# Performance work log

Measured on AMD Instinct MI355X. Metric: run time of the kernel, lower is better.

Reference implementation:

```python
import jax, jax.numpy as jnp
import numpy as np

BETA_MEM = 0.9
BETA_INH = 0.6
THRESHOLD = 1.0  # snn.Leaky default


def setup_inputs() -> dict:
    key = jax.random.key(0)
    k1, = jax.random.split(key, 1)
    T, B = 1024, 16384
    spike_seq = (jax.random.uniform(k1, (T, B, 2)) < 0.05).astype(jnp.float32)
    w_exc = jnp.array([[0.7, 1.0]], dtype=jnp.float32)  # fc_exc.weight, [1, 2]
    w_inh = jnp.array(-1.0, dtype=jnp.float32)          # scalar inhibitory weight
    return {"spike_seq": spike_seq, "w_exc": w_exc, "w_inh": w_inh}


@jax.custom_vjp
def spike_fn(x):
    # Heaviside spike with ATan surrogate gradient (snntorch default, alpha=2)
    return (x > 0).astype(x.dtype)

def _spike_fwd(x):
    return spike_fn(x), x

def _spike_bwd(x, g):
    return (g / (1.0 + (jnp.pi * x) ** 2),)

spike_fn.defvjp(_spike_fwd, _spike_bwd)


def reference(spike_seq, w_exc, w_inh):
    T, B, _ = spike_seq.shape
    mem0 = jnp.zeros((B, 1), dtype=spike_seq.dtype)
    inh0 = jnp.zeros((B, 1), dtype=spike_seq.dtype)

    def step(carry, x_t):
        mem, inh = carry
        cur_exc = x_t @ w_exc.T                      # [B, 1]
        fm1 = x_t[:, 0:1]                            # [B, 1]
        inh = BETA_INH * inh + fm1
        cur = cur_exc + w_inh * inh
        # snn.Leaky: reset (subtract) computed from previous mem, detached
        reset = jax.lax.stop_gradient((mem - THRESHOLD > 0).astype(mem.dtype))
        mem = BETA_MEM * mem + cur - reset * THRESHOLD
        spk = spike_fn(mem - THRESHOLD)
        return (mem, inh), (spk, mem)

    _, (spk_rec, mem_rec) = jax.lax.scan(step, (mem0, inh0), spike_seq)
    return spk_rec, mem_rec  # each [T, B, 1]
```

## Files before the change

kernel.cpp:

```cpp
#include <hip/hip_runtime.h>

#define T_LEN 1024
#define B_N   16384
#define UNROLL 16

__global__ __launch_bounds__(64, 1) void FMFMNeuronInhib_34033320854098_kernel(
    const float* __restrict__ x,
    const float* __restrict__ w_exc,
    const float* __restrict__ w_inh,
    float* __restrict__ out) {
#pragma clang fp contract(off)
  const int b = blockIdx.x * 64 + threadIdx.x;
  const float w0 = w_exc[0];
  const float w1 = w_exc[1];
  const float wi = w_inh[0];

  float* __restrict__ spk_out = out;
  float* __restrict__ mem_out = out + (size_t)T_LEN * B_N;
  const float2* __restrict__ xp = (const float2*)x;

  float mem = 0.0f;
  float inh = 0.0f;

  float2 cur_buf[UNROLL];
  float2 nxt_buf[UNROLL];

#pragma unroll
  for (int u = 0; u < UNROLL; ++u) cur_buf[u] = xp[u * B_N + b];

  for (int t0 = 0; t0 < T_LEN; t0 += UNROLL) {
    const int t1 = t0 + UNROLL;
    if (t1 < T_LEN) {
#pragma unroll
      for (int u = 0; u < UNROLL; ++u) nxt_buf[u] = xp[(t1 + u) * B_N + b];
    }
#pragma unroll
    for (int u = 0; u < UNROLL; ++u) {
      const int t = t0 + u;
      const float x0 = cur_buf[u].x;
      const float x1 = cur_buf[u].y;
      const float cur_exc = x0 * w0 + x1 * w1;
      inh = 0.6f * inh + x0;
      const float cur = cur_exc + wi * inh;
      const float reset = (mem - 1.0f > 0.0f) ? 1.0f : 0.0f;
      mem = 0.9f * mem + cur - reset * 1.0f;
      const float spk = (mem - 1.0f > 0.0f) ? 1.0f : 0.0f;
      spk_out[t * B_N + b] = spk;
      mem_out[t * B_N + b] = mem;
    }
#pragma unroll
    for (int u = 0; u < UNROLL; ++u) cur_buf[u] = nxt_buf[u];
  }
}

extern "C" void kernel_launch(void* const* d_in, const int* in_sizes, int n_in,
                              void* d_out, int out_size, void* d_ws, size_t ws_size,
                              hipStream_t stream) {
  const float* x     = (const float*)d_in[0];
  const float* w_exc = (const float*)d_in[1];
  const float* w_inh = (const float*)d_in[2];
  float* out = (float*)d_out;

  dim3 grid(B_N / 64);
  dim3 block(64);
  hipLaunchKernelGGL(FMFMNeuronInhib_34033320854098_kernel, grid, block, 0, stream,
                     x, w_exc, w_inh, out);
}
```

Baseline: 259.2 us.

## Ping-pong double-buffer input loads with sched barriers and nontemporal stores

Replaces the copy-based prefetch buffer with two alternating register buffers of 32 steps each. The loads for one half are issued before computing the other half, and scheduling barriers pin that order. Outputs are written with nontemporal stores to avoid polluting the cache. This is meant to keep more memory loads in flight per thread and drop the register copy, at the cost of higher register pressure.

```diff
diff --git a/kernel.cpp b/kernel.cpp
--- a/kernel.cpp
+++ b/kernel.cpp
@@ -2,7 +2,7 @@
 
 #define T_LEN 1024
 #define B_N   16384
-#define UNROLL 16
+#define UNROLL 32
 
 __global__ __launch_bounds__(64, 1) void FMFMNeuronInhib_34033320854098_kernel(
     const float* __restrict__ x,
@@ -17,39 +17,52 @@
 
   float* __restrict__ spk_out = out;
   float* __restrict__ mem_out = out + (size_t)T_LEN * B_N;
-  const float2* __restrict__ xp = (const float2*)x;
+  const float2* __restrict__ xp = (const float2*)x + b;
 
   float mem = 0.0f;
   float inh = 0.0f;
 
-  float2 cur_buf[UNROLL];
-  float2 nxt_buf[UNROLL];
+  auto step = [&](int t, float2 xv) {
+#pragma clang fp contract(off)
+    const float x0 = xv.x;
+    const float x1 = xv.y;
+    const float cur_exc = x0 * w0 + x1 * w1;
+    inh = 0.6f * inh + x0;
+    const float cur = cur_exc + wi * inh;
+    const float reset = (mem - 1.0f > 0.0f) ? 1.0f : 0.0f;
+    mem = 0.9f * mem + cur - reset * 1.0f;
+    const float spk = (mem - 1.0f > 0.0f) ? 1.0f : 0.0f;
+    __builtin_nontemporal_store(spk, &spk_out[(size_t)t * B_N + b]);
+    __builtin_nontemporal_store(mem, &mem_out[(size_t)t * B_N + b]);
+  };
+
+  float2 bufA[UNROLL];
+  float2 bufB[UNROLL];
 
 #pragma unroll
-  for (int u = 0; u < UNROLL; ++u) cur_buf[u] = xp[u * B_N + b];
+  for (int u = 0; u < UNROLL; ++u) bufA[u] = xp[(size_t)u * B_N];
+  __builtin_amdgcn_sched_barrier(0);
 
-  for (int t0 = 0; t0 < T_LEN; t0 += UNROLL) {
-    const int t1 = t0 + UNROLL;
-    if (t1 < T_LEN) {
+  for (int t0 = 0; t0 < T_LEN; t0 += 2 * UNROLL) {
 #pragma unroll
-      for (int u = 0; u < UNROLL; ++u) nxt_buf[u] = xp[(t1 + u) * B_N + b];
+    for (int u = 0; u < UNROLL; ++u)
+      bufB[u] = xp[(size_t)(t0 + UNROLL + u) * B_N];
+    __builtin_amdgcn_sched_barrier(0);
+
+#pragma unroll
+    for (int u = 0; u < UNROLL; ++u) step(t0 + u, bufA[u]);
+    __builtin_amdgcn_sched_barrier(0);
+
+    if (t0 + 2 * UNROLL < T_LEN) {
+#pragma unroll
+      for (int u = 0; u < UNROLL; ++u)
+        bufA[u] = xp[(size_t)(t0 + 2 * UNROLL + u) * B_N];
     }
+    __builtin_amdgcn_sched_barrier(0);
+
 #pragma unroll
-    for (int u = 0; u < UNROLL; ++u) {
-      const int t = t0 + u;
-      const float x0 = cur_buf[u].x;
-      const float x1 = cur_buf[u].y;
-      const float cur_exc = x0 * w0 + x1 * w1;
-      inh = 0.6f * inh + x0;
-      const float cur = cur_exc + wi * inh;
-      const float reset = (mem - 1.0f > 0.0f) ? 1.0f : 0.0f;
-      mem = 0.9f * mem + cur - reset * 1.0f;
-      const float spk = (mem - 1.0f > 0.0f) ? 1.0f : 0.0f;
-      spk_out[t * B_N + b] = spk;
-      mem_out[t * B_N + b] = mem;
-    }
-#pragma unroll
-    for (int u = 0; u < UNROLL; ++u) cur_buf[u] = nxt_buf[u];
+    for (int u = 0; u < UNROLL; ++u) step(t0 + UNROLL + u, bufB[u]);
+    __builtin_amdgcn_sched_barrier(0);
   }
 }
 
```

New measurement: 231.0 us. 1.12x faster.

## Warp-specialize into async LDS loader, compute, and store waves

Applied to the files above, without the earlier changes.

Splits each block into three wavefronts: one issues asynchronous global-to-LDS loads for a 4-deep ring of 16-timestep phases, one runs the sequential neuron recurrence from LDS into a double-buffered output tile, and one writes the previous phase's outputs to global memory. Barriers per phase keep the roles in lockstep. The intent is to keep more memory traffic in flight per CU and overlap loads, the serial recurrence, and stores, instead of a single wave handling all three. It adds LDS use, block-wide barriers every phase, and hand-placed waitcnt assembly that must stay matched to the issue counts.

```diff
diff --git a/kernel.cpp b/kernel.cpp
--- a/kernel.cpp
+++ b/kernel.cpp
@@ -1,55 +1,105 @@
 #include <hip/hip_runtime.h>
 
-#define T_LEN 1024
-#define B_N   16384
-#define UNROLL 16
+#define T_LEN   1024
+#define B_N     16384
+#define PH      16
+#define NPHASES (T_LEN / PH)
 
-__global__ __launch_bounds__(64, 1) void FMFMNeuronInhib_34033320854098_kernel(
+__shared__ __align__(16) float2 IN_lds[4][PH][64];
+__shared__ __align__(16) float2 OUT_lds[2][PH][64];
+
+static __device__ __forceinline__ void block_barrier() {
+  asm volatile("" ::: "memory");
+  __builtin_amdgcn_s_barrier();
+  asm volatile("" ::: "memory");
+}
+
+__global__ __launch_bounds__(192, 1) void FMFMNeuronInhib_34033320854098_kernel(
     const float* __restrict__ x,
     const float* __restrict__ w_exc,
     const float* __restrict__ w_inh,
     float* __restrict__ out) {
 #pragma clang fp contract(off)
-  const int b = blockIdx.x * 64 + threadIdx.x;
-  const float w0 = w_exc[0];
-  const float w1 = w_exc[1];
-  const float wi = w_inh[0];
+  const int lane = threadIdx.x & 63;
+  const int wid  = threadIdx.x >> 6;
+  const int nb0  = blockIdx.x * 64;
 
   float* __restrict__ spk_out = out;
   float* __restrict__ mem_out = out + (size_t)T_LEN * B_N;
-  const float2* __restrict__ xp = (const float2*)x;
 
-  float mem = 0.0f;
-  float inh = 0.0f;
-
-  float2 cur_buf[UNROLL];
-  float2 nxt_buf[UNROLL];
-
+  if (wid == 1) {
+    const int half = lane >> 5;
+    const int l32  = lane & 31;
+    auto issue_phase = [&](int q) {
 #pragma unroll
-  for (int u = 0; u < UNROLL; ++u) cur_buf[u] = xp[u * B_N + b];
-
-  for (int t0 = 0; t0 < T_LEN; t0 += UNROLL) {
-    const int t1 = t0 + UNROLL;
-    if (t1 < T_LEN) {
+      for (int j = 0; j < 8; ++j) {
+        const int t = q * PH + 2 * j + half;
+        const float* src = x + ((size_t)t * B_N + nb0) * 2 + (size_t)l32 * 4;
+        __builtin_amdgcn_global_load_lds(
+            (const __attribute__((address_space(1))) void*)src,
+            (__attribute__((address_space(3))) void*)&IN_lds[q & 3][2 * j][0],
+            16, 0, 0);
+      }
+    };
+    issue_phase(0); issue_phase(1); issue_phase(2);
+    asm volatile("s_waitcnt vmcnt(16)" ::: "memory");
+    block_barrier();
+    for (int p = 0; p < NPHASES; ++p) {
+      if (p + 3 < NPHASES) issue_phase(p + 3);
+      if (p <= NPHASES - 4)      asm volatile("s_waitcnt vmcnt(16)" ::: "memory");
+      else if (p == NPHASES - 3) asm volatile("s_waitcnt vmcnt(8)"  ::: "memory");
+      else                       asm volatile("s_waitcnt vmcnt(0)"  ::: "memory");
+      block_barrier();
+    }
+  } else if (wid == 0) {
+    const float w0 = w_exc[0];
+    const float w1 = w_exc[1];
+    const float wi = w_inh[0];
+    float mem = 0.0f, inh = 0.0f;
+    block_barrier();
+    for (int p = 0; p < NPHASES; ++p) {
+      float2 xv[PH];
 #pragma unroll
-      for (int u = 0; u < UNROLL; ++u) nxt_buf[u] = xp[(t1 + u) * B_N + b];
+      for (int u = 0; u < PH; ++u) xv[u] = IN_lds[p & 3][u][lane];
+#pragma unroll
+      for (int u = 0; u < PH; ++u) {
+        const float x0 = xv[u].x;
+        const float x1 = xv[u].y;
+        const float cur_exc = x0 * w0 + x1 * w1;
+        inh = 0.6f * inh + x0;
+        const float cur = cur_exc + wi * inh;
+        const float reset = (mem > 1.0f) ? 1.0f : 0.0f;
+        mem = 0.9f * mem + cur - reset;
+        const float spk = (mem > 1.0f) ? 1.0f : 0.0f;
+        OUT_lds[p & 1][u][lane] = make_float2(spk, mem);
+      }
+      asm volatile("s_waitcnt lgkmcnt(0)" ::: "memory");
+      block_barrier();
     }
+  } else {
+    block_barrier();
+    for (int p = 0; p < NPHASES; ++p) {
+      if (p >= 1) {
+        const int tb = (p - 1) * PH;
 #pragma unroll
-    for (int u = 0; u < UNROLL; ++u) {
-      const int t = t0 + u;
-      const float x0 = cur_buf[u].x;
-      const float x1 = cur_buf[u].y;
-      const float cur_exc = x0 * w0 + x1 * w1;
-      inh = 0.6f * inh + x0;
-      const float cur = cur_exc + wi * inh;
-      const float reset = (mem - 1.0f > 0.0f) ? 1.0f : 0.0f;
-      mem = 0.9f * mem + cur - reset * 1.0f;
-      const float spk = (mem - 1.0f > 0.0f) ? 1.0f : 0.0f;
-      spk_out[t * B_N + b] = spk;
-      mem_out[t * B_N + b] = mem;
+        for (int u = 0; u < PH; ++u) {
+          const float2 v = OUT_lds[(p - 1) & 1][u][lane];
+          const size_t idx = (size_t)(tb + u) * B_N + nb0 + lane;
+          spk_out[idx] = v.x;
+          mem_out[idx] = v.y;
+        }
+        asm volatile("s_waitcnt lgkmcnt(0)" ::: "memory");
+      }
+      block_barrier();
     }
+    const int tb = (NPHASES - 1) * PH;
 #pragma unroll
-    for (int u = 0; u < UNROLL; ++u) cur_buf[u] = nxt_buf[u];
+    for (int u = 0; u < PH; ++u) {
+      const float2 v = OUT_lds[(NPHASES - 1) & 1][u][lane];
+      const size_t idx = (size_t)(tb + u) * B_N + nb0 + lane;
+      spk_out[idx] = v.x;
+      mem_out[idx] = v.y;
+    }
   }
 }
 
@@ -62,7 +112,7 @@
   float* out = (float*)d_out;
 
   dim3 grid(B_N / 64);
-  dim3 block(64);
+  dim3 block(192);
   hipLaunchKernelGGL(FMFMNeuronInhib_34033320854098_kernel, grid, block, 0, stream,
                      x, w_exc, w_inh, out);
 }
```

Result: faster. 230.9 us (-10.9%).
